# Optimization experiments

Hardware: AMD Instinct MI355X
Metric: run time of the kernel (lower is better)

## Reference

```python
import jax, jax.numpy as jnp
import numpy as np
import math

N_HEADS = 8

def setup_inputs() -> dict:
    key = jax.random.key(0)
    ks = jax.random.split(key, 5)
    B, S, D = 2, 2048, 512
    return {
        "x": jax.random.normal(ks[0], (B, S, D), dtype=jnp.float32),
        "w_in": jax.random.normal(ks[1], (3 * D, D), dtype=jnp.float32) * (1.0 / math.sqrt(D)),
        "b_in": jax.random.normal(ks[2], (3 * D,), dtype=jnp.float32) * 0.01,
        "w_out": jax.random.normal(ks[3], (D, D), dtype=jnp.float32) * (1.0 / math.sqrt(D)),
        "b_out": jax.random.normal(ks[4], (D,), dtype=jnp.float32) * 0.01,
        "casual_mask": 1,
    }

def reference(x, w_in, b_in, w_out, b_out, casual_mask):
    B, S, D = x.shape
    H = N_HEADS
    dh = D // H
    # in_proj: torch Linear -> x @ W.T + b
    qvk = x @ w_in.T + b_in  # [B, S, 3D]
    # NOTE: source unpacks as q, v, k (chunk order quirk preserved)
    q, v, k = jnp.split(qvk, 3, axis=-1)
    # [B, S, D] -> [B, H, S, dh]
    def to_heads(t):
        return t.reshape(B, S, H, dh).transpose(0, 2, 1, 3)
    q, k, v = to_heads(q), to_heads(k), to_heads(v)
    scores = jnp.einsum("bhqd,bhkd->bhqk", q, k)  # [B, H, S, S]
    if casual_mask:
        # mask BEFORE scaling, as in the source (-inf unaffected by division)
        tri = jnp.triu(jnp.ones((S, S), dtype=bool), k=1)
        scores = jnp.where(tri, -jnp.inf, scores)
    scores = scores / math.sqrt(dh)
    attn = jax.nn.softmax(scores, axis=-1)
    out = jnp.einsum("bhqk,bhkd->bhqd", attn, v)  # [B, H, S, dh]
    out = out.transpose(0, 2, 1, 3).reshape(B, S, D)
    return out @ w_out.T + b_out
```

## Files before the change

### kernel.cpp

```cpp
#include <hip/hip_runtime.h>
#include <hip/hip_bf16.h>

typedef unsigned short u16;
typedef unsigned int u32;
typedef __attribute__((ext_vector_type(8))) short bf16x8;
typedef __attribute__((ext_vector_type(4))) short bf16x4;
typedef __attribute__((ext_vector_type(4))) float f32x4;

#define DEVI __device__ __forceinline__

DEVI u16 f2bf(float f) {
  union { float f; unsigned int u; } v; v.f = f;
  unsigned int u = v.u;
  unsigned int r = (u + 0x7fffu + ((u >> 16) & 1u)) >> 16;
  return (u16)r;
}

DEVI float fexp2(float x) {
#if __has_builtin(__builtin_amdgcn_exp2f)
  return __builtin_amdgcn_exp2f(x);
#else
  return exp2f(x);
#endif
}

DEVI void lds_cp16(u16* lds, const u16* g) {
  __builtin_amdgcn_global_load_lds(
      (const __attribute__((address_space(1))) u32*)g,
      (__attribute__((address_space(3))) u32*)lds, 16, 0, 0);
}

DEVI f32x4 mfma16x16x16_bf16(bf16x4 a, bf16x4 b, f32x4 c) {
#if __has_builtin(__builtin_amdgcn_mfma_f32_16x16x16bf16_1k)
  return __builtin_amdgcn_mfma_f32_16x16x16bf16_1k(a, b, c, 0, 0, 0);
#else
  f32x4 d;
  asm volatile("v_mfma_f32_16x16x16_bf16 %0, %1, %2, %3"
               : "=v"(d) : "v"(a), "v"(b), "v"(c));
  return d;
#endif
}

__global__ __launch_bounds__(256) void cvt_all(
    const float4* __restrict__ x, const float4* __restrict__ wi,
    const float4* __restrict__ wo, u16* __restrict__ xb,
    u16* __restrict__ wib, u16* __restrict__ wob) {
  int i = blockIdx.x * 256 + threadIdx.x;
  const float4* src; u16* dst; int off;
  if (i < 524288)      { src = x;  dst = xb;  off = i; }
  else if (i < 720896) { src = wi; dst = wib; off = i - 524288; }
  else                 { src = wo; dst = wob; off = i - 720896; }
  float4 f = src[off];
  ushort4 o;
  o.x = f2bf(f.x); o.y = f2bf(f.y); o.z = f2bf(f.z); o.w = f2bf(f.w);
  ((ushort4*)dst)[off] = o;
}

__global__ __launch_bounds__(256) void inproj_gemm(
    const u16* __restrict__ xb, const u16* __restrict__ wb,
    const float* __restrict__ bin,
    u16* __restrict__ Qb, u16* __restrict__ Kb, u16* __restrict__ Vrow) {
  const int K = 512;
  __shared__ u16 At[2][64 * 32];
  __shared__ u16 Bt[2][128 * 32];
  int tid = threadIdx.x;
  int w = tid >> 6, lane = tid & 63;
  int ql = lane & 15, quad = lane >> 4;
  int wr = w >> 1, wc = w & 1;
  int mtile = blockIdx.x * 64, ntile = blockIdx.y * 128;

  int r4 = lane >> 2, c4 = lane & 3;
  int swz4 = c4 ^ (r4 & 3);

  const u16* ag0 = xb + (size_t)(mtile + w * 16 + r4) * K + swz4 * 8;
  const u16* bg0 = wb + (size_t)(ntile + w * 32 + r4) * K + swz4 * 8;

  f32x4 acc[2][4];
#pragma unroll
  for (int t = 0; t < 2; ++t)
#pragma unroll
    for (int u = 0; u < 4; ++u) acc[t][u] = (f32x4){0, 0, 0, 0};

  lds_cp16(&At[0][w * 512], ag0);
  lds_cp16(&Bt[0][w * 1024], bg0);
  lds_cp16(&Bt[0][w * 1024 + 512], bg0 + 16 * K);

  int cb = ql & 3;
  for (int kk = 0; kk < 16; ++kk) {
    int cur = kk & 1;
    __syncthreads();
    if (kk < 15) {
      int k0 = (kk + 1) * 32;
      lds_cp16(&At[cur ^ 1][w * 512], ag0 + k0);
      lds_cp16(&Bt[cur ^ 1][w * 1024], bg0 + k0);
      lds_cp16(&Bt[cur ^ 1][w * 1024 + 512], bg0 + 16 * K + k0);
    }
    bf16x8 af[2], bf[4];
#pragma unroll
    for (int t = 0; t < 2; ++t) {
      int row = wr * 32 + t * 16 + ql;
      af[t] = *(const bf16x8*)(&At[cur][row * 32 + ((quad ^ cb) * 8)]);
    }
#pragma unroll
    for (int u = 0; u < 4; ++u) {
      int row = wc * 64 + u * 16 + ql;
      bf[u] = *(const bf16x8*)(&Bt[cur][row * 32 + ((quad ^ cb) * 8)]);
    }
#pragma unroll
    for (int t = 0; t < 2; ++t)
#pragma unroll
      for (int u = 0; u < 4; ++u)
        acc[t][u] = __builtin_amdgcn_mfma_f32_16x16x32_bf16(af[t], bf[u], acc[t][u], 0, 0, 0);
  }

#pragma unroll
  for (int u = 0; u < 4; ++u) {
    int n = ntile + wc * 64 + u * 16 + ql;
    float bias = bin[n];
    int chunk = n >> 9;
    int nc = n & 511;
    int h = nc >> 6, d = nc & 63;
#pragma unroll
    for (int t = 0; t < 2; ++t)
#pragma unroll
      for (int r = 0; r < 4; ++r) {
        int m = mtile + wr * 32 + t * 16 + quad * 4 + r;
        int b = m >> 11, s = m & 2047;
        u16 val = f2bf(acc[t][u][r] + bias);
        size_t idx = (((size_t)(b * 8 + h)) * 2048 + s) * 64 + d;
        if (chunk == 0)      Qb[idx] = val;
        else if (chunk == 2) Kb[idx] = val;
        else                 Vrow[idx] = val;
      }
  }
}

__global__ __launch_bounds__(256) void transpose_v(
    const u16* __restrict__ Vrow, u16* __restrict__ Vt) {
  __shared__ u16 T[64][68];
  int tid = threadIdx.x;
  int stile = blockIdx.x, bh = blockIdx.y;
  const u16* src = Vrow + ((size_t)bh * 2048 + stile * 64) * 64;
  int r = tid >> 3, c = (tid & 7) * 8;
  *(bf16x8*)&T[r][c]      = *(const bf16x8*)(src + r * 64 + c);
  *(bf16x8*)&T[r + 32][c] = *(const bf16x8*)(src + (r + 32) * 64 + c);
  __syncthreads();
  u16* dst = Vt + (size_t)bh * 64 * 2048 + stile * 64;
#pragma unroll
  for (int p = 0; p < 2; ++p) {
    int oc = p * 256 + tid;
    int d = oc >> 3, sc = (oc & 7) * 8;
    union { bf16x8 v; u16 e[8]; } out;
#pragma unroll
    for (int i = 0; i < 8; ++i) out.e[i] = T[sc + i][d];
    *(bf16x8*)(dst + (size_t)d * 2048 + sc) = out.v;
  }
}

__global__ __launch_bounds__(512) void attn_kernel(
    const u16* __restrict__ Qb, const u16* __restrict__ Kb,
    const u16* __restrict__ Vt, u16* __restrict__ Ob) {
  const int S = 2048;
  __shared__ u16 Kt[2][2][4096];
  __shared__ u16 Vl[2][2][4096];
  int tid = threadIdx.x;
  int grp = tid >> 8;
  int w = (tid >> 6) & 3;
  int lane = tid & 63;
  int ql = lane & 15, quad = lane >> 4;
  int j = blockIdx.x;
  int tileA = j, tileB = 31 - j;
  int bh = blockIdx.y;
  int qbaseA = tileA * 64 + w * 16;
  int qbaseB = tileB * 64 + w * 16;
  const u16* Qh = Qb + (size_t)bh * S * 64;
  const u16* Kh = Kb + (size_t)bh * S * 64;
  const u16* Vh = Vt + (size_t)bh * 64 * S;

  int r8 = lane >> 3, c8 = lane & 7;
  int swz = c8 ^ r8;
  int cb = ql & 7;
  const float SCL = 0.180336878f;

  bf16x8 qA0 = *(const bf16x8*)(Qh + (size_t)(qbaseA + ql) * 64 + quad * 8);
  bf16x8 qA1 = *(const bf16x8*)(Qh + (size_t)(qbaseA + ql) * 64 + 32 + quad * 8);
  bf16x8 qB0 = *(const bf16x8*)(Qh + (size_t)(qbaseB + ql) * 64 + quad * 8);
  bf16x8 qB1 = *(const bf16x8*)(Qh + (size_t)(qbaseB + ql) * 64 + 32 + quad * 8);

  f32x4 oA[4] = {{0,0,0,0},{0,0,0,0},{0,0,0,0},{0,0,0,0}};
  f32x4 oB[4] = {{0,0,0,0},{0,0,0,0},{0,0,0,0},{0,0,0,0}};
  float mA = -3.0e38f, lA = 0.0f, mB = -3.0e38f, lB = 0.0f;

  auto stage = [&](int buf, int kbase) {
    const u16* kg = Kh + (size_t)(kbase + w * 16 + r8) * 64 + swz * 8;
    lds_cp16(&Kt[grp][buf][w * 1024], kg);
    lds_cp16(&Kt[grp][buf][w * 1024 + 512], kg + 8 * 64);
    const u16* vg = Vh + (size_t)(w * 16 + r8) * S + kbase + swz * 8;
    lds_cp16(&Vl[grp][buf][w * 1024], vg);
    lds_cp16(&Vl[grp][buf][w * 1024 + 512], vg + 8 * S);
  };
  auto process = [&](int cur, int kbase, int qbase, bf16x8 x0, bf16x8 x1,
                     f32x4 (&o)[4], float& m, float& l) {
    int q = qbase + ql;
    f32x4 st[4];
#pragma unroll
    for (int t = 0; t < 4; ++t) {
      const u16* kr = &Kt[grp][cur][(t * 16 + ql) * 64];
      bf16x8 kf0 = *(const bf16x8*)(kr + ((quad ^ cb) * 8));
      bf16x8 kf1 = *(const bf16x8*)(kr + (((quad + 4) ^ cb) * 8));
      f32x4 s = {0, 0, 0, 0};
      s = __builtin_amdgcn_mfma_f32_16x16x32_bf16(kf0, x0, s, 0, 0, 0);
      s = __builtin_amdgcn_mfma_f32_16x16x32_bf16(kf1, x1, s, 0, 0, 0);
      st[t] = s;
    }
    bool needmask = (kbase + 63 > qbase);
    float sc[4][4];
#pragma unroll
    for (int t = 0; t < 4; ++t)
#pragma unroll
      for (int r = 0; r < 4; ++r) {
        float v = st[t][r] * SCL;
        if (needmask) {
          int key = kbase + t * 16 + quad * 4 + r;
          if (key > q) v = -3.0e38f;
        }
        sc[t][r] = v;
      }
    float mx = sc[0][0];
#pragma unroll
    for (int t = 0; t < 4; ++t)
#pragma unroll
      for (int r = 0; r < 4; ++r) mx = fmaxf(mx, sc[t][r]);
    mx = fmaxf(mx, __shfl_xor(mx, 16));
    mx = fmaxf(mx, __shfl_xor(mx, 32));
    float mn = fmaxf(m, mx);
    float alpha = fexp2(m - mn);
    m = mn;
    float rs = 0.0f;
    bf16x4 p[4];
#pragma unroll
    for (int t = 0; t < 4; ++t)
#pragma unroll
      for (int r = 0; r < 4; ++r) {
        float e = fexp2(sc[t][r] - mn);
        rs += e;
        p[t][r] = (short)f2bf(e);
      }
    rs += __shfl_xor(rs, 16);
    rs += __shfl_xor(rs, 32);
    l = l * alpha + rs;
#pragma unroll
    for (int d = 0; d < 4; ++d) o[d] *= alpha;
#pragma unroll
    for (int t = 0; t < 4; ++t)
#pragma unroll
      for (int d = 0; d < 4; ++d) {
        const u16* vr = &Vl[grp][cur][(d * 16 + ql) * 64];
        bf16x4 vf = *(const bf16x4*)(vr + (((t * 2 + (quad >> 1)) ^ cb) * 8 + (quad & 1) * 4));
        o[d] = mfma16x16x16_bf16(vf, p[t], o[d]);
      }
  };

  {
    int i0 = grp * 17;
    int kb = (i0 <= tileA) ? i0 : (i0 - tileA - 1);
    stage(0, kb * 64);
  }

  for (int r = 0; r < 17; ++r) {
    int i = grp * 17 + r;
    int cur = r & 1;
    __syncthreads();
    int inext = i + 1;
    if (r + 1 < 17 && inext < 33) {
      int kb = (inext <= tileA) ? inext : (inext - tileA - 1);
      stage(cur ^ 1, kb * 64);
    }
    if (i < 33) {
      if (i <= tileA) process(cur, i * 64, qbaseA, qA0, qA1, oA, mA, lA);
      else            process(cur, (i - tileA - 1) * 64, qbaseB, qB0, qB1, oB, mB, lB);
    }
  }

  float* ob  = (float*)&Kt[0][0][0];
  float* mlb = (float*)&Vl[0][0][0];
  int lg = tid & 255;
  int b = bh >> 3, h = bh & 7;
  __syncthreads();
  if (grp == 1) {
#pragma unroll
    for (int d = 0; d < 4; ++d)
#pragma unroll
      for (int r = 0; r < 4; ++r) ob[lg * 16 + d * 4 + r] = oB[d][r];
    mlb[lg * 2] = mB;
    mlb[lg * 2 + 1] = lB;
  }
  __syncthreads();
  if (grp == 0) {
    float invA = 1.0f / lA;
    size_t rowA = ((size_t)b * 2048 + qbaseA + ql) * 512 + h * 64;
#pragma unroll
    for (int d = 0; d < 4; ++d) {
      ushort4 v;
      v.x = f2bf(oA[d][0] * invA);
      v.y = f2bf(oA[d][1] * invA);
      v.z = f2bf(oA[d][2] * invA);
      v.w = f2bf(oA[d][3] * invA);
      *(ushort4*)(Ob + rowA + d * 16 + quad * 4) = v;
    }
    float mBo = mlb[lg * 2], lBo = mlb[lg * 2 + 1];
    float M = fmaxf(mB, mBo);
    float a0 = fexp2(mB - M), a1 = fexp2(mBo - M);
    float L = lB * a0 + lBo * a1;
    float inv = 1.0f / L;
    size_t rowB = ((size_t)b * 2048 + qbaseB + ql) * 512 + h * 64;
#pragma unroll
    for (int d = 0; d < 4; ++d) {
      ushort4 v;
      v.x = f2bf((oB[d][0] * a0 + ob[lg * 16 + d * 4 + 0] * a1) * inv);
      v.y = f2bf((oB[d][1] * a0 + ob[lg * 16 + d * 4 + 1] * a1) * inv);
      v.z = f2bf((oB[d][2] * a0 + ob[lg * 16 + d * 4 + 2] * a1) * inv);
      v.w = f2bf((oB[d][3] * a0 + ob[lg * 16 + d * 4 + 3] * a1) * inv);
      *(ushort4*)(Ob + rowB + d * 16 + quad * 4) = v;
    }
  }
}

__global__ __launch_bounds__(256) void outproj_gemm(
    const u16* __restrict__ Ob, const u16* __restrict__ wb,
    const float* __restrict__ bout, float* __restrict__ out) {
  const int K = 512;
  __shared__ u16 At[2][64 * 32];
  __shared__ u16 Bt[2][128 * 32];
  int tid = threadIdx.x;
  int w = tid >> 6, lane = tid & 63;
  int ql = lane & 15, quad = lane >> 4;
  int wr = w >> 1, wc = w & 1;
  int mtile = blockIdx.x * 64, ntile = blockIdx.y * 128;

  int r4 = lane >> 2, c4 = lane & 3;
  int swz4 = c4 ^ (r4 & 3);

  const u16* ag0 = Ob + (size_t)(mtile + w * 16 + r4) * K + swz4 * 8;
  const u16* bg0 = wb + (size_t)(ntile + w * 32 + r4) * K + swz4 * 8;

  f32x4 acc[2][4];
#pragma unroll
  for (int t = 0; t < 2; ++t)
#pragma unroll
    for (int u = 0; u < 4; ++u) acc[t][u] = (f32x4){0, 0, 0, 0};

  lds_cp16(&At[0][w * 512], ag0);
  lds_cp16(&Bt[0][w * 1024], bg0);
  lds_cp16(&Bt[0][w * 1024 + 512], bg0 + 16 * K);

  int cb = ql & 3;
  for (int kk = 0; kk < 16; ++kk) {
    int cur = kk & 1;
    __syncthreads();
    if (kk < 15) {
      int k0 = (kk + 1) * 32;
      lds_cp16(&At[cur ^ 1][w * 512], ag0 + k0);
      lds_cp16(&Bt[cur ^ 1][w * 1024], bg0 + k0);
      lds_cp16(&Bt[cur ^ 1][w * 1024 + 512], bg0 + 16 * K + k0);
    }
    bf16x8 af[2], bf[4];
#pragma unroll
    for (int t = 0; t < 2; ++t) {
      int row = wr * 32 + t * 16 + ql;
      af[t] = *(const bf16x8*)(&At[cur][row * 32 + ((quad ^ cb) * 8)]);
    }
#pragma unroll
    for (int u = 0; u < 4; ++u) {
      int row = wc * 64 + u * 16 + ql;
      bf[u] = *(const bf16x8*)(&Bt[cur][row * 32 + ((quad ^ cb) * 8)]);
    }
#pragma unroll
    for (int t = 0; t < 2; ++t)
#pragma unroll
      for (int u = 0; u < 4; ++u)
        acc[t][u] = __builtin_amdgcn_mfma_f32_16x16x32_bf16(af[t], bf[u], acc[t][u], 0, 0, 0);
  }

#pragma unroll
  for (int u = 0; u < 4; ++u) {
    int n = ntile + wc * 64 + u * 16 + ql;
    float bias = bout[n];
#pragma unroll
    for (int t = 0; t < 2; ++t)
#pragma unroll
      for (int r = 0; r < 4; ++r) {
        int mm = mtile + wr * 32 + t * 16 + quad * 4 + r;
        out[(size_t)mm * 512 + n] = acc[t][u][r] + bias;
      }
  }
}

extern "C" void kernel_launch(void* const* d_in, const int* in_sizes, int n_in,
                              void* d_out, int out_size, void* d_ws, size_t ws_size,
                              hipStream_t stream) {
  const float* x     = (const float*)d_in[0];
  const float* w_in  = (const float*)d_in[1];
  const float* b_in  = (const float*)d_in[2];
  const float* w_out = (const float*)d_in[3];
  const float* b_out = (const float*)d_in[4];
  float* out = (float*)d_out;
  char* ws = (char*)d_ws;

  u16* xb    = (u16*)(ws);
  u16* winb  = (u16*)(ws + 4194304);
  u16* woutb = (u16*)(ws + 5767168);
  u16* Qb    = (u16*)(ws + 6291456);
  u16* Kb    = (u16*)(ws + 10485760);
  u16* Vt    = (u16*)(ws + 14680064);
  u16* Ob    = (u16*)(ws + 18874368);
  u16* Vrow  = Ob;

  cvt_all<<<3072, 256, 0, stream>>>((const float4*)x, (const float4*)w_in,
                                    (const float4*)w_out, xb, winb, woutb);
  inproj_gemm<<<dim3(64, 12), 256, 0, stream>>>(xb, winb, b_in, Qb, Kb, Vrow);
  transpose_v<<<dim3(32, 16), 256, 0, stream>>>(Vrow, Vt);
  attn_kernel<<<dim3(16, 16), 512, 0, stream>>>(Qb, Kb, Vt, Ob);
  outproj_gemm<<<dim3(64, 4), 256, 0, stream>>>(Ob, woutb, b_out, out);
}
```

Measured before the change: 135.5 us.

## Fuse V transpose into in-projection epilogue and enlarge GEMM M tile

The in-projection GEMM now writes V directly in transposed [bh, d, s] layout, which removes the separate transpose_v kernel launch and its extra global read and write of V. The GEMM M tile is also doubled from 64 to 128 rows, so each block computes 4x4 MFMA tiles and the grid drops to 32x12 blocks. The transposed stores are scattered 2-byte writes with stride 2048, which could coalesce poorly. The larger tile raises register use and halves the number of blocks.

```diff
diff --git a/kernel.cpp b/kernel.cpp
--- a/kernel.cpp
+++ b/kernel.cpp
@@ -59,29 +59,30 @@
 __global__ __launch_bounds__(256) void inproj_gemm(
     const u16* __restrict__ xb, const u16* __restrict__ wb,
     const float* __restrict__ bin,
-    u16* __restrict__ Qb, u16* __restrict__ Kb, u16* __restrict__ Vrow) {
+    u16* __restrict__ Qb, u16* __restrict__ Kb, u16* __restrict__ Vt) {
   const int K = 512;
-  __shared__ u16 At[2][64 * 32];
+  __shared__ u16 At[2][128 * 32];
   __shared__ u16 Bt[2][128 * 32];
   int tid = threadIdx.x;
   int w = tid >> 6, lane = tid & 63;
   int ql = lane & 15, quad = lane >> 4;
   int wr = w >> 1, wc = w & 1;
-  int mtile = blockIdx.x * 64, ntile = blockIdx.y * 128;
+  int mtile = blockIdx.x * 128, ntile = blockIdx.y * 128;
 
   int r4 = lane >> 2, c4 = lane & 3;
   int swz4 = c4 ^ (r4 & 3);
 
-  const u16* ag0 = xb + (size_t)(mtile + w * 16 + r4) * K + swz4 * 8;
+  const u16* ag0 = xb + (size_t)(mtile + w * 32 + r4) * K + swz4 * 8;
   const u16* bg0 = wb + (size_t)(ntile + w * 32 + r4) * K + swz4 * 8;
 
-  f32x4 acc[2][4];
-#pragma unroll
-  for (int t = 0; t < 2; ++t)
+  f32x4 acc[4][4];
+#pragma unroll
+  for (int t = 0; t < 4; ++t)
 #pragma unroll
     for (int u = 0; u < 4; ++u) acc[t][u] = (f32x4){0, 0, 0, 0};
 
-  lds_cp16(&At[0][w * 512], ag0);
+  lds_cp16(&At[0][w * 1024], ag0);
+  lds_cp16(&At[0][w * 1024 + 512], ag0 + 16 * K);
   lds_cp16(&Bt[0][w * 1024], bg0);
   lds_cp16(&Bt[0][w * 1024 + 512], bg0 + 16 * K);
 
@@ -91,14 +92,15 @@
     __syncthreads();
     if (kk < 15) {
       int k0 = (kk + 1) * 32;
-      lds_cp16(&At[cur ^ 1][w * 512], ag0 + k0);
+      lds_cp16(&At[cur ^ 1][w * 1024], ag0 + k0);
+      lds_cp16(&At[cur ^ 1][w * 1024 + 512], ag0 + 16 * K + k0);
       lds_cp16(&Bt[cur ^ 1][w * 1024], bg0 + k0);
       lds_cp16(&Bt[cur ^ 1][w * 1024 + 512], bg0 + 16 * K + k0);
     }
-    bf16x8 af[2], bf[4];
-#pragma unroll
-    for (int t = 0; t < 2; ++t) {
-      int row = wr * 32 + t * 16 + ql;
+    bf16x8 af[4], bf[4];
+#pragma unroll
+    for (int t = 0; t < 4; ++t) {
+      int row = wr * 64 + t * 16 + ql;
       af[t] = *(const bf16x8*)(&At[cur][row * 32 + ((quad ^ cb) * 8)]);
     }
 #pragma unroll
@@ -107,7 +109,7 @@
       bf[u] = *(const bf16x8*)(&Bt[cur][row * 32 + ((quad ^ cb) * 8)]);
     }
 #pragma unroll
-    for (int t = 0; t < 2; ++t)
+    for (int t = 0; t < 4; ++t)
 #pragma unroll
       for (int u = 0; u < 4; ++u)
         acc[t][u] = __builtin_amdgcn_mfma_f32_16x16x32_bf16(af[t], bf[u], acc[t][u], 0, 0, 0);
@@ -121,39 +123,17 @@
     int nc = n & 511;
     int h = nc >> 6, d = nc & 63;
 #pragma unroll
-    for (int t = 0; t < 2; ++t)
+    for (int t = 0; t < 4; ++t)
 #pragma unroll
       for (int r = 0; r < 4; ++r) {
-        int m = mtile + wr * 32 + t * 16 + quad * 4 + r;
+        int m = mtile + wr * 64 + t * 16 + quad * 4 + r;
         int b = m >> 11, s = m & 2047;
         u16 val = f2bf(acc[t][u][r] + bias);
-        size_t idx = (((size_t)(b * 8 + h)) * 2048 + s) * 64 + d;
-        if (chunk == 0)      Qb[idx] = val;
-        else if (chunk == 2) Kb[idx] = val;
-        else                 Vrow[idx] = val;
+        int bh = b * 8 + h;
+        if (chunk == 0)      Qb[((size_t)bh * 2048 + s) * 64 + d] = val;
+        else if (chunk == 2) Kb[((size_t)bh * 2048 + s) * 64 + d] = val;
+        else                 Vt[((size_t)bh * 64 + d) * 2048 + s] = val;
       }
-  }
-}
-
-__global__ __launch_bounds__(256) void transpose_v(
-    const u16* __restrict__ Vrow, u16* __restrict__ Vt) {
-  __shared__ u16 T[64][68];
-  int tid = threadIdx.x;
-  int stile = blockIdx.x, bh = blockIdx.y;
-  const u16* src = Vrow + ((size_t)bh * 2048 + stile * 64) * 64;
-  int r = tid >> 3, c = (tid & 7) * 8;
-  *(bf16x8*)&T[r][c]      = *(const bf16x8*)(src + r * 64 + c);
-  *(bf16x8*)&T[r + 32][c] = *(const bf16x8*)(src + (r + 32) * 64 + c);
-  __syncthreads();
-  u16* dst = Vt + (size_t)bh * 64 * 2048 + stile * 64;
-#pragma unroll
-  for (int p = 0; p < 2; ++p) {
-    int oc = p * 256 + tid;
-    int d = oc >> 3, sc = (oc & 7) * 8;
-    union { bf16x8 v; u16 e[8]; } out;
-#pragma unroll
-    for (int i = 0; i < 8; ++i) out.e[i] = T[sc + i][d];
-    *(bf16x8*)(dst + (size_t)d * 2048 + sc) = out.v;
   }
 }
 
@@ -414,12 +394,10 @@
   u16* Kb    = (u16*)(ws + 10485760);
   u16* Vt    = (u16*)(ws + 14680064);
   u16* Ob    = (u16*)(ws + 18874368);
-  u16* Vrow  = Ob;
 
   cvt_all<<<3072, 256, 0, stream>>>((const float4*)x, (const float4*)w_in,
                                     (const float4*)w_out, xb, winb, woutb);
-  inproj_gemm<<<dim3(64, 12), 256, 0, stream>>>(xb, winb, b_in, Qb, Kb, Vrow);
-  transpose_v<<<dim3(32, 16), 256, 0, stream>>>(Vrow, Vt);
+  inproj_gemm<<<dim3(32, 12), 256, 0, stream>>>(xb, winb, b_in, Qb, Kb, Vt);
   attn_kernel<<<dim3(16, 16), 512, 0, stream>>>(Qb, Kb, Vt, Ob);
   outproj_gemm<<<dim3(64, 4), 256, 0, stream>>>(Ob, woutb, b_out, out);
 }
```

Result: no change. 135.9 us (+0.3%).
